# Kernel tuning notes

Measured on AMD Instinct MI355X. Metric: run time of the kernel, lower is better.

The kernel has to match this reference:

```python
import jax, jax.numpy as jnp
import numpy as np

N_CLASSES = 10   # number of distinct private-attribute labels
DIM = 16         # PCA / GMM dimension (init arg `dim`)
SIGMA = 1.0      # init arg `sigma`, cov = sigma * I


def _pca(X, k):
    # torch PCA: center, SVD of X^T, project onto first k left singular vectors
    X = X - jnp.mean(X, axis=0)
    U, _, _ = jnp.linalg.svd(X.T, full_matrices=False)  # U: [D, min(D,B)]
    return X @ U[:, :k]                                  # [B, k]


def _gmm_loss(x, labels):
    # x: [B, k] PCA-projected features, labels: [B] int class ids in [0, C)
    B = x.shape[0]
    dtype = x.dtype
    ones = jnp.ones((B,), dtype)
    counts = jax.ops.segment_sum(ones, labels, num_segments=N_CLASSES)          # [C]
    sums = jax.ops.segment_sum(x, labels, num_segments=N_CLASSES)               # [C, k]
    safe = jnp.maximum(counts, 1.0)
    means = sums / safe[:, None]                                                # [C, k]

    diff = x - means[labels]                                                    # [B, k]
    outers = diff[:, :, None] * diff[:, None, :]                                # [B, k, k]
    Ssum = jax.ops.segment_sum(outers, labels, num_segments=N_CLASSES)          # [C, k, k]
    Sigma = SIGMA * jnp.eye(DIM, dtype=dtype) + Ssum / safe[:, None, None]      # [C, k, k]

    inv = jnp.linalg.inv(Sigma)                                                 # [C, k, k]
    _, logdet = jnp.linalg.slogdet(Sigma)                                       # [C]

    # KL(N_i || N_j) = 0.5*(tr(S_j^-1 S_i) + (u_j-u_i)^T S_j^-1 (u_j-u_i) - k + logdet_j - logdet_i)
    tr = jnp.einsum('jab,iba->ij', inv, Sigma)                                  # [C, C]
    d = means[None, :, :] - means[:, None, :]                                   # d[i,j] = u_j - u_i
    maha = jnp.einsum('ija,jab,ijb->ij', d, inv, d)                             # [C, C]
    kl = 0.5 * (tr + maha - DIM + logdet[None, :] - logdet[:, None])            # [C, C]

    present = counts > 0
    W = counts[:, None] * counts[None, :]
    mask = present[:, None] & present[None, :] & ~jnp.eye(N_CLASSES, dtype=bool)
    result = jnp.sum(jnp.where(mask, kl * W, jnp.zeros_like(kl)))
    return result / (jnp.asarray(B, dtype) ** 3)


def setup_inputs() -> dict:
    key = jax.random.key(0)
    k1, k2 = jax.random.split(key)
    mu = jax.random.normal(k1, (16384, 1024), dtype=jnp.float32)
    private_attribute = jax.random.randint(k2, (16384,), 0, N_CLASSES, dtype=jnp.int32)
    return {"mu": mu, "private_attribute": private_attribute}


def reference(mu, private_attribute):
    B = mu.shape[0]
    x = mu.reshape(B, -1)          # flatten(start_dim=1)
    x = _pca(x, DIM)               # [B, DIM]
    labels = private_attribute.astype(jnp.int32)
    return _gmm_loss(x, labels)
```

## Files before the change

kernel.cpp:

```cpp
#include <hip/hip_runtime.h>
#include <math.h>

#define BN 16384
#define DN 1024
#define CHEB_D 8

static constexpr size_t OFF_C    = 0x000000;
static constexpr size_t OFF_P    = 0x400000;
static constexpr size_t OFF_Y0   = 0x800000;
static constexpr size_t OFF_Y1   = 0x840000;
static constexpr size_t OFF_Y2   = 0x880000;
static constexpr size_t OFF_Y3   = 0x8C0000;
static constexpr size_t OFF_CQ   = 0x900000;
static constexpr size_t OFF_S64  = 0x940000;
static constexpr size_t OFF_LF   = 0x948000;
static constexpr size_t OFF_T64  = 0x950000;
static constexpr size_t OFF_V16  = 0x958000;
static constexpr size_t OFF_UT   = 0x960000;
static constexpr size_t OFF_UTT  = 0x970000;
static constexpr size_t OFF_S16  = 0x980000;
static constexpr size_t OFF_CS   = 0x980100;
static constexpr size_t OFF_TR   = 0x981100;
static constexpr size_t OFF_SCAL = 0x981200;
static constexpr size_t OFF_STAT = 0x981300;
static constexpr size_t OFF_F    = 0x990000;
static constexpr size_t OFF_M    = 0xA90000;

typedef float f32x4 __attribute__((ext_vector_type(4)));
typedef short bf16x8 __attribute__((ext_vector_type(8)));
typedef unsigned int u32x4v __attribute__((ext_vector_type(4)));

__device__ __forceinline__ float wsumf(float v){
  #pragma unroll
  for (int off=32; off; off>>=1) v += __shfl_xor(v, off, 64);
  return v;
}
__device__ __forceinline__ float wminf(float v){
  #pragma unroll
  for (int off=32; off; off>>=1) v = fminf(v, __shfl_xor(v, off, 64));
  return v;
}
__device__ __forceinline__ float wmaxf(float v){
  #pragma unroll
  for (int off=32; off; off>>=1) v = fmaxf(v, __shfl_xor(v, off, 64));
  return v;
}
__device__ __forceinline__ float lanebc(float x, int l){
  return __int_as_float(__builtin_amdgcn_readlane(__float_as_int(x), l));
}


__global__ __launch_bounds__(256) void colsum_k(const float* __restrict__ X, float* __restrict__ cs){
  int b = blockIdx.x, t = threadIdx.x;
  float a0=0.f,a1=0.f,a2=0.f,a3=0.f;
  for (int r=0; r<256; ++r){
    const float4 v = *(const float4*)(X + (size_t)(b*256 + r)*1024 + t*4);
    a0 += v.x; a1 += v.y; a2 += v.z; a3 += v.w;
  }
  atomicAdd(&cs[t*4+0], a0); atomicAdd(&cs[t*4+1], a1);
  atomicAdd(&cs[t*4+2], a2); atomicAdd(&cs[t*4+3], a3);
}

#define SYRK_SLICES 27
#define SYRK_KCHUNK 608
#define SYRKM_SLICES 4
#define SYRKM_KCHUNK 256

__device__ __forceinline__ f32x4 mfma32(bf16x8 a, bf16x8 b, f32x4 c){
  return __builtin_amdgcn_mfma_f32_16x16x32_bf16(a, b, c, 0, 0, 0);
}

template<int KCHUNK>
__device__ __forceinline__ void syrk_mfma_body(const float* __restrict__ X, float* __restrict__ G, int KMAX){
  int bx = blockIdx.x;
  int tp = bx % 36, ks = bx / 36;
  int ti = 0, rem = tp;
  while (rem >= 8 - ti){ rem -= 8 - ti; ++ti; }
  int tj = ti + rem;
  int k0 = ks * KCHUNK;
  int kend = k0 + KCHUNK; if (kend > KMAX) kend = KMAX;

  __shared__ __attribute__((aligned(16))) unsigned int LdsT[2][3][128][20];

  int t = threadIdx.x;
  int wid = t >> 6, lane = t & 63;
  int wr = wid >> 1, wc = wid & 1;
  int lm = lane & 15;
  int lk = lane >> 4;

  f32x4 acc[4][4];
  #pragma unroll
  for (int i=0;i<4;++i)
    #pragma unroll
    for (int j=0;j<4;++j) acc[i][j] = (f32x4){0.f,0.f,0.f,0.f};

  for (int kc = k0; kc < kend; kc += 32){
    __syncthreads();
    #pragma unroll
    for (int w=0; w<4; ++w){
      int job = t + 256*w;
      int c   = job & 127;
      int pk  = job >> 7;
      int p   = pk >> 2;
      int kpg = pk & 3;
      const float* src = X + (size_t)(kc + kpg*8)*1024 + (p ? tj : ti)*128 + c;
      float e[8];
      #pragma unroll
      for (int i=0;i<8;++i) e[i] = src[(size_t)i*1024];
      unsigned hh[8]; float r2f[8]; unsigned mm[8];
      #pragma unroll
      for (int i=0;i<8;++i){
        unsigned u = __float_as_uint(e[i]);
        hh[i] = u & 0xFFFF0000u;
        float r1 = e[i] - __uint_as_float(hh[i]);
        mm[i] = __float_as_uint(r1) & 0xFFFF0000u;
        r2f[i] = r1 - __uint_as_float(mm[i]);
      }
      u32x4v hp, mp, lp;
      #pragma unroll
      for (int j=0;j<4;++j){
        hp[j] = (hh[2*j] >> 16) | hh[2*j+1];
        mp[j] = (mm[2*j] >> 16) | mm[2*j+1];
        lp[j] = (__float_as_uint(r2f[2*j]) >> 16) | (__float_as_uint(r2f[2*j+1]) & 0xFFFF0000u);
      }
      *(u32x4v*)&LdsT[p][0][c][kpg*4] = hp;
      *(u32x4v*)&LdsT[p][1][c][kpg*4] = mp;
      *(u32x4v*)&LdsT[p][2][c][kpg*4] = lp;
    }
    __syncthreads();
    bf16x8 af[3][4], bg[3][4];
    #pragma unroll
    for (int fm=0; fm<4; ++fm){
      int ca = wr*64 + fm*16 + lm;
      int cb = wc*64 + fm*16 + lm;
      #pragma unroll
      for (int tm=0; tm<3; ++tm){
        af[tm][fm] = *(const bf16x8*)&LdsT[0][tm][ca][lk*4];
        bg[tm][fm] = *(const bf16x8*)&LdsT[1][tm][cb][lk*4];
      }
    }
    #pragma unroll
    for (int fm=0; fm<4; ++fm)
      #pragma unroll
      for (int fn=0; fn<4; ++fn){
        f32x4 a = acc[fm][fn];
        a = mfma32(af[0][fm], bg[0][fn], a);
        a = mfma32(af[0][fm], bg[1][fn], a);
        a = mfma32(af[1][fm], bg[0][fn], a);
        a = mfma32(af[0][fm], bg[2][fn], a);
        a = mfma32(af[2][fm], bg[0][fn], a);
        a = mfma32(af[1][fm], bg[1][fn], a);
        acc[fm][fn] = a;
      }
  }
  #pragma unroll
  for (int fm=0; fm<4; ++fm){
    int gi = ti*128 + wr*64 + fm*16 + lk*4;
    #pragma unroll
    for (int fn=0; fn<4; ++fn){
      int gj = tj*128 + wc*64 + fn*16 + lm;
      #pragma unroll
      for (int rg=0; rg<4; ++rg)
        atomicAdd(&G[(size_t)(gi+rg)*1024 + gj], acc[fm][fn][rg]);
    }
  }
}

__global__ __launch_bounds__(256, 2) void syrk_mfma_k(const float* __restrict__ X, float* __restrict__ G){
  syrk_mfma_body<SYRK_KCHUNK>(X, G, 16384);
}
__global__ __launch_bounds__(256, 2) void syrkM_mfma_k(const float* __restrict__ X, float* __restrict__ G){
  syrk_mfma_body<SYRKM_KCHUNK>(X, G, 1024);
}

__global__ __launch_bounds__(256) void trace_k(const float* __restrict__ G, const float* __restrict__ cs,
                                               float* __restrict__ scal){
  __shared__ float red[4];
  int t = threadIdx.x;
  float s = 0.f;
  #pragma unroll
  for (int w=0; w<4; ++w){
    int i = t + 256*w;
    float d = cs[i];
    s += G[(size_t)i*1025] - d*d*(1.0f/16384.0f);
  }
  s = wsumf(s);
  if ((t & 63) == 0) red[t >> 6] = s;
  __syncthreads();
  if (t == 0){
    float trD = (red[0]+red[1]+red[2]+red[3]) * (1.0f/1024.0f);
    float c = 1.40f * trD, a = 0.25f * trD;
    scal[0] = 0.5f*(c + a);
    scal[1] = 2.0f/(c - a);
  }
}

__global__ __launch_bounds__(256) void formCChat_k(float* __restrict__ C, const float* __restrict__ cs,
                                                   const float* __restrict__ scal){
  int g = blockIdx.x*256 + threadIdx.x;
  int i = g >> 10, j = g & 1023;
  if (j < i) return;
  float mid = scal[0], ie = scal[1];
  float v = C[g] - cs[i]*cs[j]*(1.0f/16384.0f);
  float h = ie*(v - ((i==j) ? mid : 0.f));
  C[g] = h;
  C[j*1024 + i] = h;
}

__global__ __launch_bounds__(256) void formM_k(float* __restrict__ M){
  int g = blockIdx.x*256 + threadIdx.x;
  int i = g >> 10, j = g & 1023;
  if (j < i) return;
  float v = 2.f*M[g] - ((i==j) ? 1.f : 0.f);
  M[g] = v;
  M[j*1024 + i] = v;
}

__global__ void rng_k(float* __restrict__ Y){
  int idx = blockIdx.x*256 + threadIdx.x;
  unsigned h = (unsigned)idx * 2654435761u;
  h ^= h >> 16; h *= 2246822519u; h ^= h >> 13; h *= 3266489917u; h ^= h >> 16;
  Y[idx] = (float)(h & 0xFFFFFFu) * (2.0f/16777216.0f) - 1.0f;
}

__global__ __launch_bounds__(256) void mv_k(const float* __restrict__ Yt, const float* __restrict__ Cm, float* __restrict__ P){
  int bx = blockIdx.x;
  int nt = bx & 15, ks = bx >> 4;
  int n0 = nt*64, k0 = ks*64;
  __shared__ __attribute__((aligned(16))) float At[64][68];
  __shared__ __attribute__((aligned(16))) float Bt[64][68];
  int t = threadIdx.x;
  #pragma unroll
  for (int w=0; w<4; ++w){
    int job = t + 256*w;
    int m  = job >> 4, f4 = job & 15;
    float4 v = *(const float4*)(Yt + (size_t)m*1024 + k0 + f4*4);
    At[f4*4+0][m] = v.x; At[f4*4+1][m] = v.y; At[f4*4+2][m] = v.z; At[f4*4+3][m] = v.w;
    int kk = job >> 4, fn = job & 15;
    *(float4*)&Bt[kk][fn*4] = *(const float4*)(Cm + (size_t)(k0+kk)*1024 + n0 + fn*4);
  }
  __syncthreads();
  int tm = t & 15, tn = t >> 4;
  float acc[4][4];
  #pragma unroll
  for (int i=0;i<4;++i)
    #pragma unroll
    for (int j=0;j<4;++j) acc[i][j]=0.f;
  for (int kk=0; kk<64; ++kk){
    float4 a = *(const float4*)&At[kk][tm*4];
    float4 b = *(const float4*)&Bt[kk][tn*4];
    float av[4] = {a.x,a.y,a.z,a.w};
    float bv[4] = {b.x,b.y,b.z,b.w};
    #pragma unroll
    for (int i=0;i<4;++i)
      #pragma unroll
      for (int j=0;j<4;++j) acc[i][j] += av[i]*bv[j];
  }
  #pragma unroll
  for (int i=0;i<4;++i){
    float4 o; o.x=acc[i][0]; o.y=acc[i][1]; o.z=acc[i][2]; o.w=acc[i][3];
    *(float4*)(P + (size_t)(ks*64 + tm*4 + i)*1024 + n0 + tn*4) = o;
  }
}

__global__ __launch_bounds__(256) void combine_k(const float* __restrict__ P, const float* __restrict__ Tk1,
                                                 float* __restrict__ out, int mode){
  int idx = (blockIdx.x*256 + threadIdx.x)*4;
  float s0=0.f,s1=0.f,s2=0.f,s3=0.f;
  #pragma unroll
  for (int ks=0; ks<16; ++ks){
    const float4 p = *(const float4*)(P + (size_t)ks*65536 + idx);
    s0 += p.x; s1 += p.y; s2 += p.z; s3 += p.w;
  }
  float4 o;
  if (mode == 0){
    o.x=s0; o.y=s1; o.z=s2; o.w=s3;
  } else {
    const float4 t1 = *(const float4*)(Tk1 + idx);
    o.x = 2.f*s0 - t1.x; o.y = 2.f*s1 - t1.y;
    o.z = 2.f*s2 - t1.z; o.w = 2.f*s3 - t1.w;
  }
  *(float4*)(out+idx) = o;
}

__global__ __launch_bounds__(256) void gram_k(const float* __restrict__ A, const float* __restrict__ Bm, double* __restrict__ S){
  int bx = blockIdx.x;
  int i = bx >> 2, jg = bx & 3;
  __shared__ __attribute__((aligned(16))) float Ai[1024];
  __shared__ double red[16][17];
  int t = threadIdx.x;
  ((float4*)Ai)[t] = ((const float4*)(A + (size_t)i*1024))[t];
  __syncthreads();
  int jl = t >> 4, kp = t & 15;
  const float* Br = Bm + (size_t)(jg*16 + jl)*1024 + kp*64;
  const float* Ar = Ai + kp*64;
  double acc = 0.0;
  #pragma unroll 8
  for (int kk=0; kk<64; ++kk) acc += (double)Br[kk] * (double)Ar[kk];
  red[jl][kp] = acc;
  __syncthreads();
  if (t < 16){
    double s = 0.0;
    #pragma unroll
    for (int p2=0; p2<16; ++p2) s += red[t][p2];
    S[i*64 + jg*16 + t] = s;
  }
}

__global__ __launch_bounds__(64) void chol_k(const double* __restrict__ S, float* __restrict__ Lf){
  __shared__ double L[64][65];
  __shared__ double col[64];
  int t = threadIdx.x;
  for (int e=t; e<4096; e+=64) L[e>>6][e&63] = S[e];
  __syncthreads();
  for (int k=0; k<64; ++k){
    double lkk = sqrt(fmax(L[k][k], 1e-280));
    double r = 1.0/lkk;
    double ck = (t > k) ? L[t][k]*r : 0.0;
    col[t] = ck;
    if (t == k) L[k][k] = lkk;
    if (t > k)  L[t][k] = ck;
    __syncthreads();
    #pragma unroll
    for (int j=0; j<64; j+=8){
      L[t][j+0] -= ck*col[j+0];
      L[t][j+1] -= ck*col[j+1];
      L[t][j+2] -= ck*col[j+2];
      L[t][j+3] -= ck*col[j+3];
      L[t][j+4] -= ck*col[j+4];
      L[t][j+5] -= ck*col[j+5];
      L[t][j+6] -= ck*col[j+6];
      L[t][j+7] -= ck*col[j+7];
    }
    __syncthreads();
  }
  for (int e=t; e<4096; e+=64){
    int i = e >> 6, j = e & 63;
    Lf[e] = (j < i) ? (float)L[i][j] : ((j == i) ? (float)(1.0/L[i][i]) : 0.f);
  }
}

__global__ __launch_bounds__(256) void applysolve_k(const float* __restrict__ Yin, const float* __restrict__ Lf, float* __restrict__ Qout){
  int k = blockIdx.x*256 + threadIdx.x;
  float z[64];
  #pragma unroll
  for (int c=0; c<64; ++c){
    float v = Yin[(size_t)c*1024 + k];
    #pragma unroll
    for (int j=0; j<c; ++j) v -= Lf[c*64+j]*z[j];
    z[c] = v * Lf[c*64+c];
  }
  #pragma unroll
  for (int c=0; c<64; ++c) Qout[(size_t)c*1024 + k] = z[c];
}

__global__ __launch_bounds__(256) void eig16_k(const double* __restrict__ Tin, float* __restrict__ V16){
  __shared__ float A[64][65];
  __shared__ float pp[4][64];
  __shared__ float dF[64], eF[64], e2F[64], kapS[64];
  __shared__ float lamF[16];
  __shared__ float IV[5][64][16];
  __shared__ float W[16][68];
  int t = threadIdx.x;
  int r = t & 63, p4 = t >> 6;
  int j0 = p4*16;

  for (int e=t; e<4096; e+=256){
    int i = e >> 6, j = e & 63;
    A[i][j] = (float)(0.5*(Tin[i*64+j] + Tin[(size_t)j*64+i]));
  }
  __syncthreads();

  for (int k=0; k<62; ++k){
    float ckreg = A[r][k];
    float ck = (r > k) ? ckreg : 0.f;
    float sig = wsumf(ck*ck);
    float x1 = lanebc(ckreg, k+1);
    float rr = sqrtf(sig);
    float alpha = (x1 >= 0.f) ? -rr : rr;
    float kappa = sig - alpha*x1;
    float kinv = (kappa > 1e-30f) ? 1.f/kappa : 0.f;
    float vown = ck;
    if (r == k+1) vown = x1 - alpha;
    if (kinv == 0.f) vown = 0.f;
    if (t == 0){ eF[k] = (kinv==0.f) ? 0.f : alpha; kapS[k] = (kinv==0.f) ? 0.f : kappa; }
    float vj[16];
    #pragma unroll
    for (int jj=0; jj<16; ++jj){
      int j = j0 + jj;
      float cj = lanebc(ckreg, j);
      float vv = (j > k) ? cj : 0.f;
      if (j == k+1) vv = x1 - alpha;
      if (kinv == 0.f) vv = 0.f;
      vj[jj] = vv;
    }
    float prt = 0.f;
    #pragma unroll
    for (int jj=0; jj<16; ++jj) prt += A[r][j0+jj]*vj[jj];
    pp[p4][r] = prt;
    __syncthreads();
    float pfull = pp[0][r] + pp[1][r] + pp[2][r] + pp[3][r];
    float pi = (r > k) ? pfull*kinv : 0.f;
    float vp = wsumf(vown*pi);
    float Kc = vp*0.5f*kinv;
    float qown = (r > k) ? (pi - Kc*vown) : 0.f;
    #pragma unroll
    for (int jj=0; jj<16; ++jj){
      int j = j0 + jj;
      float qj = lanebc(qown, j);
      float aold = A[r][j];
      float anew = aold - (vown*qj + qown*vj[jj]);
      if (j == k) anew = (r > k) ? vown : aold;
      A[r][j] = anew;
    }
    __syncthreads();
  }

  if (t < 64) dF[t] = A[t][t];
  if (t == 0){ eF[62] = A[63][62]; eF[63] = 0.f; kapS[62] = 0.f; kapS[63] = 0.f; }
  __syncthreads();
  if (t < 64) e2F[t] = eF[t]*eF[t];
  __syncthreads();

  float em1 = (r > 0) ? fabsf(eF[r-1]) : 0.f;
  float ep  = fabsf(eF[r]);
  float glo = wminf(dF[r] - em1 - ep);
  float ghi = wmaxf(dF[r] + em1 + ep);
  float span = ghi - glo + 1.f;
  float lo = glo - 0.001f*span, hi = ghi + 0.001f*span;

  int eidx = t >> 4, g = t & 15;
  int m = 48 + eidx;
  for (int it=0; it<7; ++it){
    float x = lo + (hi - lo)*((float)(g+1)*(1.0f/17.0f));
    float qq = dF[0] - x;
    int c = (qq < 0.f) ? 1 : 0;
    #pragma unroll
    for (int j=1; j<64; ++j){
      float aq = fabsf(qq);
      float qs = (aq < 1e-10f) ? ((qq < 0.f) ? -1e-10f : 1e-10f) : qq;
      qq = dF[j] - x - e2F[j-1]*__builtin_amdgcn_rcpf(qs);
      c += (qq < 0.f) ? 1 : 0;
    }
    float cl = (c <= m) ? x : -3.4e38f;
    float ch = (c >  m) ? x :  3.4e38f;
    #pragma unroll
    for (int off=1; off<16; off<<=1){
      cl = fmaxf(cl, __shfl_xor(cl, off, 64));
      ch = fminf(ch, __shfl_xor(ch, off, 64));
    }
    lo = fmaxf(lo, cl);
    hi = fminf(hi, ch);
  }
  if (g == 0) lamF[eidx] = 0.5f*(lo + hi);
  __syncthreads();

  if (t < 16){
    float lam = lamF[t];
    const float PIVF = 1e-6f;
    #pragma unroll 4
    for (int i=0; i<64; ++i){
      unsigned hsh = (unsigned)(i*131 + t*1009 + 7);
      hsh ^= hsh >> 13; hsh *= 2654435761u; hsh ^= hsh >> 16;
      IV[4][i][t] = (float)(hsh & 0xFFFF) * (1.5f/65536.0f) + 0.25f;
    }
    unsigned long long piv = 0ull;
    float dcur = dF[0] - lam;
    float ducur = eF[0];
    for (int i=0; i<63; ++i){
      float dli = eF[i];
      float dnext = dF[i+1] - lam;
      float eip1 = (i < 62) ? eF[i+1] : 0.f;
      bool sw = fabsf(dcur) < fabsf(dli);
      float dd = dcur;
      if (fabsf(dd) < PIVF) dd = (dd < 0.f) ? -PIVF : PIVF;
      float f = sw ? (dcur*__builtin_amdgcn_rcpf(dli)) : (dli*__builtin_amdgcn_rcpf(dd));
      float ddst = sw ? dli : dd;
      float dust = sw ? dnext : ducur;
      float du2  = sw ? eip1 : 0.f;
      float dnew = sw ? (ducur - f*dnext) : (dnext - f*ducur);
      float dunew= sw ? (-f*eip1) : eip1;
      if (sw) piv |= (1ull << i);
      IV[0][i][t] = f;
      float dc = ddst; if (fabsf(dc) < PIVF) dc = (dc < 0.f) ? -PIVF : PIVF;
      IV[1][i][t] = __builtin_amdgcn_rcpf(dc);
      IV[2][i][t] = dust;
      IV[3][i][t] = du2;
      dcur = dnew; ducur = dunew;
    }
    { float dc = dcur; if (fabsf(dc) < PIVF) dc = (dc < 0.f) ? -PIVF : PIVF; IV[1][63][t] = __builtin_amdgcn_rcpf(dc); }
    float ss = 0.f;
    #pragma unroll 1
    for (int iter=0; iter<2; ++iter){
      float scale = (iter == 0) ? 1.f : rsqrtf(fmaxf(ss, 1e-30f));
      float b = IV[4][0][t]*scale;
      #pragma unroll 7
      for (int i=0; i<63; ++i){
        float bn = IV[4][i+1][t]*scale;
        float f = IV[0][i][t];
        bool sw = (piv >> i) & 1ull;
        float keep = sw ? bn : b;
        float bnew = (sw ? b : bn) - f*keep;
        IV[4][i][t] = keep;
        b = bnew;
      }
      ss = 0.f;
      float x1v = b * IV[1][63][t];
      IV[4][63][t] = x1v; ss += x1v*x1v;
      float x0v = (IV[4][62][t] - IV[2][62][t]*x1v) * IV[1][62][t];
      IV[4][62][t] = x0v; ss += x0v*x0v;
      float xp1 = x0v, xp2 = x1v;
      #pragma unroll 7
      for (int i=61; i>=0; --i){
        float xi = (IV[4][i][t] - IV[2][i][t]*xp1 - IV[3][i][t]*xp2) * IV[1][i][t];
        IV[4][i][t] = xi; ss += xi*xi;
        xp2 = xp1; xp1 = xi;
      }
    }
    #pragma unroll 4
    for (int i=0; i<64; ++i) W[t][i] = IV[4][i][t];
  }
  __syncthreads();

  for (int c=0; c<16; ++c){
    float wi = (t < 64) ? W[c][t] : 0.f;
    float s2 = wsumf(wi*wi);
    float rn = rsqrtf(fmaxf(s2, 1e-30f));
    wi *= rn;
    if (t < 64) W[c][t] = wi;
    __syncthreads();
    for (int c2=c+1; c2<16; ++c2){
      float w2 = (t < 64) ? W[c2][t] : 0.f;
      float d2 = wsumf(wi*w2);
      if (t < 64) W[c2][t] -= d2*wi;
    }
    __syncthreads();
  }

  int cL = (p4 << 2) + (r >> 4);
  int part = r & 15;
  for (int k=61; k>=0; --k){
    float kpd = kapS[k];
    if (kpd == 0.f) continue;
    float invk = 1.f/kpd;
    float vv[4];
    float ps = 0.f;
    #pragma unroll
    for (int mm=0; mm<4; ++mm){
      int i = part*4 + mm;
      vv[mm] = (i > k) ? A[i][k] : 0.f;
      ps += vv[mm]*W[cL][i];
    }
    ps += __shfl_xor(ps, 1, 64);
    ps += __shfl_xor(ps, 2, 64);
    ps += __shfl_xor(ps, 4, 64);
    ps += __shfl_xor(ps, 8, 64);
    float sc = ps * invk;
    #pragma unroll
    for (int mm=0; mm<4; ++mm){
      int i = part*4 + mm;
      W[cL][i] -= vv[mm]*sc;
    }
  }
  __syncthreads();

  for (int e=t; e<1024; e+=256){
    int j = e >> 4, c = e & 15;
    V16[e] = W[c][j];
  }
}

__global__ __launch_bounds__(256) void buildUt_k(const float* __restrict__ V16,
                                                 const float* __restrict__ Qt, float* __restrict__ Ut, float* __restrict__ UtT){
  int bx = blockIdx.x;
  int c = bx & 15, kc = bx >> 4;
  int k = kc*256 + threadIdx.x;
  float acc = 0.f;
  #pragma unroll
  for (int j=0; j<64; ++j) acc += V16[j*16 + c] * Qt[(size_t)j*1024 + k];
  Ut[(size_t)c*1024 + k] = acc;
  UtT[(size_t)k*16 + c] = acc;
}

__global__ void s16_k(const float* __restrict__ cs, const float* __restrict__ Ut, float* __restrict__ s16){
  __shared__ float red[16][17];
  int t = threadIdx.x;
  int c = t & 15, part = t >> 4;
  float acc = 0.f;
  for (int d=0; d<64; ++d) acc += cs[part*64 + d] * Ut[(size_t)c*1024 + part*64 + d];
  red[c][part] = acc;
  __syncthreads();
  if (t < 16){
    float s = 0.f;
    #pragma unroll
    for (int p2=0; p2<16; ++p2) s += red[t][p2];
    s16[t] = s * (1.0f/16384.0f);
  }
}

__global__ __launch_bounds__(256) void proj_k(const float* __restrict__ X, const float* __restrict__ UtT,
                                              const float* __restrict__ s16, float* __restrict__ F){
  int r0 = blockIdx.x * 64;
  int t = threadIdx.x;
  __shared__ __attribute__((aligned(16))) float uts[16384];
  #pragma unroll
  for (int w=0; w<16; ++w)
    ((float4*)uts)[t + 256*w] = ((const float4*)UtT)[t + 256*w];
  __syncthreads();
  int row = t & 63, kp = t >> 6;
  const float* xr = X + (size_t)(r0 + row)*1024 + kp*256;
  const float* ut = uts + kp*256*16;
  float acc[16];
  #pragma unroll
  for (int c=0;c<16;++c) acc[c] = 0.f;
  for (int dd=0; dd<256; dd+=4){
    float4 xv4 = *(const float4*)(xr + dd);
    float xv[4] = {xv4.x, xv4.y, xv4.z, xv4.w};
    #pragma unroll
    for (int u=0; u<4; ++u)
      #pragma unroll
      for (int c=0;c<16;++c) acc[c] += xv[u] * ut[(dd+u)*16 + c];
  }
  __shared__ float part[4][64][16];
  #pragma unroll
  for (int c=0;c<16;++c) part[kp][row][c] = acc[c];
  __syncthreads();
  int cq = t >> 6;
  #pragma unroll
  for (int ccx=0; ccx<4; ++ccx){
    int c = cq*4 + ccx;
    float v = part[0][row][c] + part[1][row][c] + part[2][row][c] + part[3][row][c] - s16[c];
    F[(size_t)(r0 + row)*16 + c] = v;
  }
}

__global__ __launch_bounds__(256) void stats_k(const float* __restrict__ F, const int* __restrict__ lbl, float* __restrict__ SG){
  __shared__ float st[10][154];
  int t = threadIdx.x;
  for (int e=t; e<1540; e+=256) st[e/154][e%154] = 0.f;
  __syncthreads();
  int r = blockIdx.x*256 + t;
  float f[16];
  #pragma unroll
  for (int w=0; w<4; ++w){
    float4 v = *(const float4*)(F + (size_t)r*16 + w*4);
    f[w*4+0]=v.x; f[w*4+1]=v.y; f[w*4+2]=v.z; f[w*4+3]=v.w;
  }
  int c = lbl[r];
  if ((unsigned)c < 10u){
    float* bs = &st[c][0];
    atomicAdd(&bs[0], 1.f);
    #pragma unroll
    for (int a=0;a<16;++a) atomicAdd(&bs[1+a], f[a]);
    int sidx = 17;
    #pragma unroll
    for (int a=0;a<16;++a)
      #pragma unroll
      for (int b2=a;b2<16;++b2) atomicAdd(&bs[sidx++], f[a]*f[b2]);
  }
  __syncthreads();
  for (int e=t; e<1530; e+=256) atomicAdd(&SG[e], st[e/153][e%153]);
}

__global__ __launch_bounds__(256) void final_k(const float* __restrict__ SG, float* __restrict__ out){
  __shared__ double cnt[10], safe[10], ldet[10];
  __shared__ double mean[10][16];
  __shared__ double Sig[10][16][16];
  __shared__ double Inv[10][16][16];
  __shared__ double red[128];
  int t = threadIdx.x;
  if (t < 10){
    double c0 = (double)SG[t*153];
    cnt[t] = c0; safe[t] = (c0 > 0.0) ? c0 : 1.0;
  }
  __syncthreads();
  for (int e=t; e<160; e+=256){
    int c = e >> 4, a = e & 15;
    mean[c][a] = (double)SG[c*153 + 1 + a] / safe[c];
  }
  __syncthreads();
  for (int e=t; e<2560; e+=256){
    int c = e >> 8, ab = e & 255, a = ab >> 4, b2 = ab & 15;
    int lo = a < b2 ? a : b2, hi = a < b2 ? b2 : a;
    int ti = lo*(33 - lo)/2 + (hi - lo);
    Sig[c][a][b2] = (double)SG[c*153 + 17 + ti]/safe[c] - mean[c][a]*mean[c][b2] + ((a==b2)?1.0:0.0);
  }
  __syncthreads();
  if (t < 10){
    for (int a=0;a<16;++a)
      for (int b2=0;b2<16;++b2) Inv[t][a][b2] = Sig[t][a][b2];
    double ld2 = 0.0;
    for (int k=0;k<16;++k){
      double v = Inv[t][k][k];
      for (int j=0;j<k;++j) v -= Inv[t][k][j]*Inv[t][k][j];
      v = fmax(v, 1e-280);
      double lkk = sqrt(v);
      Inv[t][k][k] = lkk; ld2 += log(lkk);
      for (int i=k+1;i<16;++i){
        double w = Inv[t][i][k];
        for (int j=0;j<k;++j) w -= Inv[t][i][j]*Inv[t][k][j];
        Inv[t][i][k] = w / lkk;
      }
    }
    ldet[t] = 2.0*ld2;
    for (int j=0;j<16;++j){
      double dj = 1.0 / Inv[t][j][j];
      Inv[t][j][j] = dj;
      for (int i=j+1;i<16;++i){
        double ssum = Inv[t][i][j]*dj;
        for (int k=j+1;k<i;++k) ssum += Inv[t][i][k]*Inv[t][k][j];
        Inv[t][i][j] = -ssum / Inv[t][i][i];
      }
    }
    double dg[16];
    #pragma unroll
    for (int a=0;a<16;++a){
      double s2 = 0.0;
      for (int k=a;k<16;++k){ double x = Inv[t][k][a]; s2 += x*x; }
      dg[a] = s2;
    }
    for (int a=0;a<16;++a)
      for (int b2=a+1;b2<16;++b2){
        double s2 = 0.0;
        for (int k=b2;k<16;++k) s2 += Inv[t][k][a]*Inv[t][k][b2];
        Inv[t][a][b2] = s2;
      }
    for (int a=0;a<16;++a) Inv[t][a][a] = dg[a];
    for (int a=0;a<16;++a)
      for (int b2=a+1;b2<16;++b2) Inv[t][b2][a] = Inv[t][a][b2];
  }
  __syncthreads();
  double contrib = 0.0;
  if (t < 100){
    int i = t/10, j = t%10;
    if (i != j && cnt[i] > 0.0 && cnt[j] > 0.0){
      double tr = 0.0;
      for (int a=0;a<16;++a)
        for (int b2=0;b2<16;++b2) tr += Inv[j][a][b2]*Sig[i][b2][a];
      double dm[16];
      #pragma unroll
      for (int a=0;a<16;++a) dm[a] = mean[j][a] - mean[i][a];
      double mah = 0.0;
      for (int a=0;a<16;++a){
        double rs = 0.0;
        for (int b2=0;b2<16;++b2) rs += Inv[j][a][b2]*dm[b2];
        mah += dm[a]*rs;
      }
      double kl = 0.5*(tr + mah - 16.0 + ldet[j] - ldet[i]);
      contrib = kl * cnt[i]*cnt[j];
    }
  }
  if (t < 128) red[t] = contrib;
  __syncthreads();
  for (int off=64; off>0; off >>= 1){
    if (t < off) red[t] += red[t+off];
    __syncthreads();
  }
  if (t == 0) out[0] = (float)(red[0] / (16384.0*16384.0*16384.0));
}

extern "C" void kernel_launch(void* const* d_in, const int* in_sizes, int n_in,
                              void* d_out, int out_size, void* d_ws, size_t ws_size,
                              hipStream_t stream){
  (void)in_sizes; (void)n_in; (void)out_size; (void)ws_size;
  const float* X  = (const float*)d_in[0];
  const int* lbl  = (const int*)d_in[1];
  char* ws = (char*)d_ws;
  float*  C    = (float*)(ws + OFF_C);
  float*  Mm   = (float*)(ws + OFF_M);
  float*  P    = (float*)(ws + OFF_P);
  float*  Y0   = (float*)(ws + OFF_Y0);
  float*  Y1   = (float*)(ws + OFF_Y1);
  float*  Y2   = (float*)(ws + OFF_Y2);
  float*  Y3   = (float*)(ws + OFF_Y3);
  float*  CQ   = (float*)(ws + OFF_CQ);
  double* S64  = (double*)(ws + OFF_S64);
  float*  LF   = (float*)(ws + OFF_LF);
  double* T64  = (double*)(ws + OFF_T64);
  float*  V16  = (float*)(ws + OFF_V16);
  float*  UT   = (float*)(ws + OFF_UT);
  float*  UTT  = (float*)(ws + OFF_UTT);
  float*  S16  = (float*)(ws + OFF_S16);
  float*  CS   = (float*)(ws + OFF_CS);
  float*  SCAL = (float*)(ws + OFF_SCAL);
  float*  STAT = (float*)(ws + OFF_STAT);
  float*  F    = (float*)(ws + OFF_F);
  float*  OUT  = (float*)d_out;

  hipMemsetAsync(C, 0, 4*1024*1024, stream);
  hipMemsetAsync(Mm, 0, 4*1024*1024, stream);
  hipMemsetAsync(ws + OFF_CS, 0, 12800, stream);

  colsum_k<<<64, 256, 0, stream>>>(X, CS);
  syrk_mfma_k<<<36*SYRK_SLICES, 256, 0, stream>>>(X, C);
  trace_k<<<1, 256, 0, stream>>>(C, CS, SCAL);
  formCChat_k<<<4096, 256, 0, stream>>>(C, CS, SCAL);
  syrkM_mfma_k<<<36*SYRKM_SLICES, 256, 0, stream>>>(C, Mm);
  formM_k<<<4096, 256, 0, stream>>>(Mm);
  rng_k<<<256, 256, 0, stream>>>(Y0);

  auto cheb = [&](float* in, float* z0, float* z1, float* z2) -> float* {
    float* bufs[3] = {z0, z1, z2};
    float* prev = in;
    float* cur = in;
    for (int s=0; s<CHEB_D; ++s){
      float* dst = bufs[s % 3];
      mv_k<<<256, 256, 0, stream>>>(cur, Mm, P);
      combine_k<<<64, 256, 0, stream>>>(P, prev, dst, (s == 0) ? 0 : 1);
      prev = cur; cur = dst;
    }
    return cur;
  };
  auto cholqr = [&](float* Yin, float* Qout){
    gram_k<<<256, 256, 0, stream>>>(Yin, Yin, S64);
    chol_k<<<1, 64, 0, stream>>>(S64, LF);
    applysolve_k<<<4, 256, 0, stream>>>(Yin, LF, Qout);
  };

  float* f1 = cheb(Y0, Y1, Y2, Y3);
  cholqr(f1, Y0);
  float* f2 = cheb(Y0, Y1, Y2, Y3);
  cholqr(f2, Y1);
  cholqr(Y1, Y3);

  mv_k<<<256, 256, 0, stream>>>(Y3, Mm, P);
  combine_k<<<64, 256, 0, stream>>>(P, Y3, CQ, 0);
  gram_k<<<256, 256, 0, stream>>>(Y3, CQ, T64);
  eig16_k<<<1, 256, 0, stream>>>(T64, V16);
  buildUt_k<<<64, 256, 0, stream>>>(V16, Y3, UT, UTT);

  s16_k<<<1, 256, 0, stream>>>(CS, UT, S16);
  proj_k<<<256, 256, 0, stream>>>(X, UTT, S16, F);
  stats_k<<<64, 256, 0, stream>>>(F, lbl, STAT);
  final_k<<<1, 256, 0, stream>>>(STAT, OUT);
}
```

Measured before the change: 1.265 ms.

## Precompute T8 via matrix squaring and run Householder tridiagonalization in registers on one wave

The degree-8 Chebyshev filter was applied as eight matrix-vector passes. It is replaced by three repeated-squaring steps on the 1024x1024 operator (syrkM plus formM, giving T2, T4, T8) followed by two matvec passes per filter application. In eig16_k, the Householder tridiagonalization now keeps each row in registers on a single wave, uses shared vectors instead of per-step block syncs, and switches to a DPP-based wave reduction. The squaring adds three full-matrix GEMMs and could amplify rounding error in exchange for fewer dependent launches and a shorter serial eigen phase.

```diff
diff --git a/kernel.cpp b/kernel.cpp
--- a/kernel.cpp
+++ b/kernel.cpp
@@ -3,7 +3,6 @@
 
 #define BN 16384
 #define DN 1024
-#define CHEB_D 8
 
 static constexpr size_t OFF_C    = 0x000000;
 static constexpr size_t OFF_P    = 0x400000;
@@ -48,6 +47,14 @@
 __device__ __forceinline__ float lanebc(float x, int l){
   return __int_as_float(__builtin_amdgcn_readlane(__float_as_int(x), l));
 }
+__device__ __forceinline__ float wred64(float x){
+  x += __int_as_float(__builtin_amdgcn_update_dpp(0, __float_as_int(x), 0x118, 0xf, 0xf, true));
+  x += __int_as_float(__builtin_amdgcn_update_dpp(0, __float_as_int(x), 0x114, 0xf, 0xf, true));
+  x += __int_as_float(__builtin_amdgcn_update_dpp(0, __float_as_int(x), 0x112, 0xf, 0xf, true));
+  x += __int_as_float(__builtin_amdgcn_update_dpp(0, __float_as_int(x), 0x111, 0xf, 0xf, true));
+  float s0 = lanebc(x, 15), s1 = lanebc(x, 31), s2 = lanebc(x, 47), s3 = lanebc(x, 63);
+  return (s0 + s1) + (s2 + s3);
+}
 
 
 __global__ __launch_bounds__(256) void colsum_k(const float* __restrict__ X, float* __restrict__ cs){
@@ -356,14 +363,14 @@
 
 __global__ __launch_bounds__(256) void eig16_k(const double* __restrict__ Tin, float* __restrict__ V16){
   __shared__ float A[64][65];
-  __shared__ float pp[4][64];
+  __shared__ __attribute__((aligned(16))) float vS[64];
+  __shared__ __attribute__((aligned(16))) float qS[64];
   __shared__ float dF[64], eF[64], e2F[64], kapS[64];
   __shared__ float lamF[16];
   __shared__ float IV[5][64][16];
   __shared__ float W[16][68];
   int t = threadIdx.x;
   int r = t & 63, p4 = t >> 6;
-  int j0 = p4*16;
 
   for (int e=t; e<4096; e+=256){
     int i = e >> 6, j = e & 63;
@@ -371,53 +378,62 @@
   }
   __syncthreads();
 
-  for (int k=0; k<62; ++k){
-    float ckreg = A[r][k];
-    float ck = (r > k) ? ckreg : 0.f;
-    float sig = wsumf(ck*ck);
-    float x1 = lanebc(ckreg, k+1);
-    float rr = sqrtf(sig);
-    float alpha = (x1 >= 0.f) ? -rr : rr;
-    float kappa = sig - alpha*x1;
-    float kinv = (kappa > 1e-30f) ? 1.f/kappa : 0.f;
-    float vown = ck;
-    if (r == k+1) vown = x1 - alpha;
-    if (kinv == 0.f) vown = 0.f;
-    if (t == 0){ eF[k] = (kinv==0.f) ? 0.f : alpha; kapS[k] = (kinv==0.f) ? 0.f : kappa; }
-    float vj[16];
-    #pragma unroll
-    for (int jj=0; jj<16; ++jj){
-      int j = j0 + jj;
-      float cj = lanebc(ckreg, j);
-      float vv = (j > k) ? cj : 0.f;
-      if (j == k+1) vv = x1 - alpha;
-      if (kinv == 0.f) vv = 0.f;
-      vj[jj] = vv;
-    }
-    float prt = 0.f;
-    #pragma unroll
-    for (int jj=0; jj<16; ++jj) prt += A[r][j0+jj]*vj[jj];
-    pp[p4][r] = prt;
-    __syncthreads();
-    float pfull = pp[0][r] + pp[1][r] + pp[2][r] + pp[3][r];
-    float pi = (r > k) ? pfull*kinv : 0.f;
-    float vp = wsumf(vown*pi);
-    float Kc = vp*0.5f*kinv;
-    float qown = (r > k) ? (pi - Kc*vown) : 0.f;
-    #pragma unroll
-    for (int jj=0; jj<16; ++jj){
-      int j = j0 + jj;
-      float qj = lanebc(qown, j);
-      float aold = A[r][j];
-      float anew = aold - (vown*qj + qown*vj[jj]);
-      if (j == k) anew = (r > k) ? vown : aold;
-      A[r][j] = anew;
-    }
-    __syncthreads();
-  }
-
-  if (t < 64) dF[t] = A[t][t];
-  if (t == 0){ eF[62] = A[63][62]; eF[63] = 0.f; kapS[62] = 0.f; kapS[63] = 0.f; }
+  if (p4 == 0){
+    float a[64];
+    #pragma unroll
+    for (int j=0; j<64; ++j) a[j] = A[r][j];
+    float ck = a[0];
+    #pragma unroll 1
+    for (int k=0; k<62; ++k){
+      int kp1 = k + 1;
+      bool below = (r > k);
+      float ckm = below ? ck : 0.f;
+      float sig = wred64(ckm*ckm);
+      float x1 = __int_as_float(__builtin_amdgcn_readlane(__float_as_int(ck), kp1));
+      float rr = sqrtf(sig);
+      float alpha = (x1 >= 0.f) ? -rr : rr;
+      float kappa = sig - alpha*x1;
+      float kinv = (kappa > 1e-30f) ? 1.f/kappa : 0.f;
+      float v = ckm;
+      if (r == kp1) v = x1 - alpha;
+      if (kinv == 0.f) v = 0.f;
+      if (r == 0){ eF[k] = (kinv==0.f) ? 0.f : alpha; kapS[k] = (kinv==0.f) ? 0.f : kappa; }
+      if (r == k) dF[k] = ck;
+      if (below) A[r][k] = v;
+      vS[r] = v;
+      float p0=0.f,p1=0.f,p2=0.f,p3=0.f;
+      #pragma unroll
+      for (int j=0; j<64; j+=4){
+        const float4 vb = *(const float4*)&vS[j];
+        p0 += a[j+0]*vb.x; p1 += a[j+1]*vb.y;
+        p2 += a[j+2]*vb.z; p3 += a[j+3]*vb.w;
+      }
+      float pf = (p0+p1)+(p2+p3);
+      float pi = below ? pf*kinv : 0.f;
+      float vp = wred64(v*pi);
+      float Kc = vp*0.5f*kinv;
+      float q = below ? (pi - Kc*v) : 0.f;
+      qS[r] = q;
+      float ckn = 0.f;
+      #pragma unroll
+      for (int j=0; j<64; j+=4){
+        const float4 vb = *(const float4*)&vS[j];
+        const float4 qb = *(const float4*)&qS[j];
+        a[j+0] -= v*qb.x + q*vb.x;
+        a[j+1] -= v*qb.y + q*vb.y;
+        a[j+2] -= v*qb.z + q*vb.z;
+        a[j+3] -= v*qb.w + q*vb.w;
+        if (j+0 == kp1) ckn = a[j+0];
+        if (j+1 == kp1) ckn = a[j+1];
+        if (j+2 == kp1) ckn = a[j+2];
+        if (j+3 == kp1) ckn = a[j+3];
+      }
+      ck = ckn;
+    }
+    if (r == 62) dF[62] = ck;
+    if (r == 63){ eF[62] = ck; dF[63] = a[63]; }
+    if (r == 0){ eF[63] = 0.f; kapS[62] = 0.f; kapS[63] = 0.f; }
+  }
   __syncthreads();
   if (t < 64) e2F[t] = eF[t]*eF[t];
   __syncthreads();
@@ -524,14 +540,14 @@
 
   for (int c=0; c<16; ++c){
     float wi = (t < 64) ? W[c][t] : 0.f;
-    float s2 = wsumf(wi*wi);
+    float s2 = wred64(wi*wi);
     float rn = rsqrtf(fmaxf(s2, 1e-30f));
     wi *= rn;
     if (t < 64) W[c][t] = wi;
     __syncthreads();
     for (int c2=c+1; c2<16; ++c2){
       float w2 = (t < 64) ? W[c2][t] : 0.f;
-      float d2 = wsumf(wi*w2);
+      float d2 = wred64(wi*w2);
       if (t < 64) W[c2][t] -= d2*wi;
     }
     __syncthreads();
@@ -797,19 +813,19 @@
   formCChat_k<<<4096, 256, 0, stream>>>(C, CS, SCAL);
   syrkM_mfma_k<<<36*SYRKM_SLICES, 256, 0, stream>>>(C, Mm);
   formM_k<<<4096, 256, 0, stream>>>(Mm);
+  hipMemsetAsync(P, 0, 4*1024*1024, stream);
+  syrkM_mfma_k<<<36*SYRKM_SLICES, 256, 0, stream>>>(Mm, P);
+  formM_k<<<4096, 256, 0, stream>>>(P);
+  hipMemsetAsync(C, 0, 4*1024*1024, stream);
+  syrkM_mfma_k<<<36*SYRKM_SLICES, 256, 0, stream>>>(P, C);
+  formM_k<<<4096, 256, 0, stream>>>(C);
   rng_k<<<256, 256, 0, stream>>>(Y0);
 
-  auto cheb = [&](float* in, float* z0, float* z1, float* z2) -> float* {
-    float* bufs[3] = {z0, z1, z2};
-    float* prev = in;
-    float* cur = in;
-    for (int s=0; s<CHEB_D; ++s){
-      float* dst = bufs[s % 3];
-      mv_k<<<256, 256, 0, stream>>>(cur, Mm, P);
-      combine_k<<<64, 256, 0, stream>>>(P, prev, dst, (s == 0) ? 0 : 1);
-      prev = cur; cur = dst;
-    }
-    return cur;
+  auto cheb2 = [&](float* U, float* Wb, float* Ob){
+    mv_k<<<256, 256, 0, stream>>>(U, C, P);
+    combine_k<<<64, 256, 0, stream>>>(P, U, Wb, 0);
+    mv_k<<<256, 256, 0, stream>>>(Wb, C, P);
+    combine_k<<<64, 256, 0, stream>>>(P, U, Ob, 1);
   };
   auto cholqr = [&](float* Yin, float* Qout){
     gram_k<<<256, 256, 0, stream>>>(Yin, Yin, S64);
@@ -817,10 +833,10 @@
     applysolve_k<<<4, 256, 0, stream>>>(Yin, LF, Qout);
   };
 
-  float* f1 = cheb(Y0, Y1, Y2, Y3);
-  cholqr(f1, Y0);
-  float* f2 = cheb(Y0, Y1, Y2, Y3);
-  cholqr(f2, Y1);
+  cheb2(Y0, Y1, Y2);
+  cholqr(Y2, Y0);
+  cheb2(Y0, Y1, Y2);
+  cholqr(Y2, Y1);
   cholqr(Y1, Y3);
 
   mv_k<<<256, 256, 0, stream>>>(Y3, Mm, P);
```

New measurement: 1.129 ms. -10.7%, faster.
